# Optimization experiments

Measured on AMD Instinct MI355X. Metric: run time of the kernel, lower is better.

The kernel has to match this reference:

```python
import jax, jax.numpy as jnp
import numpy as np
import math

N, E, K_ORD = 30000, 60000, 6
D, H, DQK, PE_DIM, HYPER, MAX_K = 256, 8, 256, 128, 256, 10
DH = DQK // H    # per-head qk dim (dim_qk_head)
DVH = D // H     # per-head v dim  (dim_v_head)
M = E * K_ORD + N  # incidence messages + node self-loops


def _sin_pe(max_len, d):
    pos = np.arange(max_len)[:, None].astype(np.float32)
    div = np.exp(np.arange(0, d, 2).astype(np.float32) * (-math.log(10000.0) / d))
    pe = np.zeros((max_len, d), np.float32)
    pe[:, 0::2] = np.sin(pos * div)
    pe[:, 1::2] = np.cos(pos * div)
    return jnp.asarray(pe)


def _ln(x, g, b, eps=1e-5):
    mu = x.mean(-1, keepdims=True)
    var = ((x - mu) ** 2).mean(-1, keepdims=True)
    return (x - mu) * jax.lax.rsqrt(var + eps) * g + b


def _mlp(x, w1, b1, w2, b2):
    return jax.nn.relu(x @ w1 + b1) @ w2 + b2


def _forward(x_v, x_e, q_w1, q_b1, q_w2, q_b2, k_w, k_b, v_w, v_b,
             m1_w1, m1_b1, m1_w2, m1_b2, m2_w1, m2_b1, m2_w2, m2_b2,
             m3_w1, m3_b1, m3_w2, m3_b2, n1_g, n1_b, n2_g, n2_b, n3_g, n3_b,
             bias_v, edge_orders, edge_index):
    n = x_v.shape[0]
    # order-conditional positional MLP residual (pe1 at order 1 for nodes, edge_orders for edges)
    pe1 = _sin_pe(MAX_K + 1, D)
    x_v = x_v + _mlp(jnp.concatenate([_ln(x_v, n1_g, n1_b), jnp.broadcast_to(pe1[1], x_v.shape)], -1), m1_w1, m1_b1, m1_w2, m1_b2)
    x_e = x_e + _mlp(jnp.concatenate([_ln(x_e, n1_g, n1_b), pe1[edge_orders]], -1), m1_w1, m1_b1, m1_w2, m1_b2)

    # queries from PositionalMLP over positions {0, 1}
    q = _mlp(_sin_pe(2, PE_DIM), q_w1, q_b1, q_w2, q_b2)  # [2, DQK]
    q0 = q[0].reshape(H, DH)
    q1 = q[1].reshape(H, DH)

    tok = jnp.concatenate([x_e, x_v], 0)                    # [E+N, D], edges first
    k_all = tok @ k_w + k_b                                  # [E+N, 2*DQK]
    k0 = k_all[:, :DQK].reshape(-1, H, DH)
    k1 = k_all[:, DQK:].reshape(-1, H, DH)
    v = (tok @ v_w + v_b).reshape(-1, H, DVH)

    # global PMA: softmax over all edge+node tokens
    logit0 = jnp.einsum('hd,ehd->eh', q0, k0) / math.sqrt(DH)
    alpha0 = jax.nn.softmax(logit0, axis=0)
    att0 = jnp.einsum('eh,ehd->hd', alpha0, v).reshape(1, D)

    # segment PMA: leaky_relu -> scatter-softmax over messages per target node
    src, tgt = edge_index[0], edge_index[1]
    a = jnp.sum(k1 * q1[None], -1)                           # [E+N, H] (no sqrt scaling, per PMA)
    a = jax.nn.leaky_relu(a[src], 0.2)                       # [M, H]
    a_max = jax.ops.segment_max(a, tgt, num_segments=n)
    a = jnp.exp(a - a_max[tgt])
    a = a / jax.ops.segment_sum(a, tgt, num_segments=n)[tgt]
    att1 = jax.ops.segment_sum(v[src] * a[..., None], tgt, num_segments=n).reshape(n, D)

    pe2 = _sin_pe(2, D)
    att0 = att0 + _mlp(jnp.concatenate([_ln(att0, n2_g, n2_b), pe2[0:1]], -1), m2_w1, m2_b1, m2_w2, m2_b2)
    att1 = att1 + _mlp(jnp.concatenate([_ln(att1, n2_g, n2_b), jnp.broadcast_to(pe2[1], att1.shape)], -1), m2_w1, m2_b1, m2_w2, m2_b2)
    x = att0 + att1
    x = x + _mlp(_ln(x, n3_g, n3_b), m3_w1, m3_b1, m3_w2, m3_b2)
    return x + bias_v


def setup_inputs():
    key = jax.random.key(0)
    ks = jax.random.split(key, 64)
    idx = iter(range(64))
    def nrm(shape, fan_in=None):
        s = 1.0 if fan_in is None else 1.0 / math.sqrt(fan_in)
        return jax.random.normal(ks[next(idx)], shape, jnp.float32) * s
    inp = {}
    inp['x_v'] = nrm((N, D))
    inp['x_e'] = nrm((E, D))
    inp['edge_orders'] = jax.random.randint(ks[next(idx)], (E,), 2, MAX_K + 1)
    tgt_inc = jax.random.randint(ks[next(idx)], (E * K_ORD,), 0, N)
    src = jnp.concatenate([jnp.repeat(jnp.arange(E), K_ORD), E + jnp.arange(N)])
    tgt = jnp.concatenate([tgt_inc, jnp.arange(N)])
    inp['edge_index'] = jnp.stack([src, tgt]).astype(jnp.int32)
    inp['q_w1'] = nrm((PE_DIM, HYPER), PE_DIM); inp['q_b1'] = jnp.zeros((HYPER,), jnp.float32)
    inp['q_w2'] = nrm((HYPER, DQK), HYPER);     inp['q_b2'] = jnp.zeros((DQK,), jnp.float32)
    inp['k_w'] = nrm((D, 2 * DQK), D);          inp['k_b'] = jnp.zeros((2 * DQK,), jnp.float32)
    inp['v_w'] = nrm((D, D), D);                inp['v_b'] = jnp.zeros((D,), jnp.float32)
    inp['m1_w1'] = nrm((2 * D, HYPER), 2 * D);  inp['m1_b1'] = jnp.zeros((HYPER,), jnp.float32)
    inp['m1_w2'] = nrm((HYPER, D), HYPER);      inp['m1_b2'] = jnp.zeros((D,), jnp.float32)
    inp['m2_w1'] = nrm((2 * D, HYPER), 2 * D);  inp['m2_b1'] = jnp.zeros((HYPER,), jnp.float32)
    inp['m2_w2'] = nrm((HYPER, D), HYPER);      inp['m2_b2'] = jnp.zeros((D,), jnp.float32)
    inp['m3_w1'] = nrm((D, HYPER), D);          inp['m3_b1'] = jnp.zeros((HYPER,), jnp.float32)
    inp['m3_w2'] = nrm((HYPER, D), HYPER);      inp['m3_b2'] = jnp.zeros((D,), jnp.float32)
    for nm in ('n1', 'n2', 'n3'):
        inp[nm + '_g'] = jnp.ones((D,), jnp.float32)
        inp[nm + '_b'] = jnp.zeros((D,), jnp.float32)
    inp['bias_v'] = jnp.zeros((D,), jnp.float32)
    return inp


def reference(x_v, x_e, edge_orders, edge_index, q_w1, q_b1, q_w2, q_b2, k_w, k_b, v_w, v_b,
              m1_w1, m1_b1, m1_w2, m1_b2, m2_w1, m2_b1, m2_w2, m2_b2,
              m3_w1, m3_b1, m3_w2, m3_b2, n1_g, n1_b, n2_g, n2_b, n3_g, n3_b, bias_v):
    return _forward(x_v, x_e, q_w1, q_b1, q_w2, q_b2, k_w, k_b, v_w, v_b,
                    m1_w1, m1_b1, m1_w2, m1_b2, m2_w1, m2_b1, m2_w2, m2_b2,
                    m3_w1, m3_b1, m3_w2, m3_b2, n1_g, n1_b, n2_g, n2_b, n3_g, n3_b,
                    bias_v, edge_orders, edge_index)
```

## Files before the change

kernel.cpp:

```cpp
#include <hip/hip_runtime.h>
#include <hip/hip_bf16.h>

#define N_NODES 30000
#define N_EDGE  60000
#define T_TOK   90000
#define M_MSG   390000
#define DD      256
#define HH      8
#define AS      260
#define A0_BLOCKS 2048
#define A0_ROWS   44
#define FUSED_BLKS 1407
#define HIST_BLKS  762

typedef unsigned short u16;
typedef unsigned int   u32;
typedef short s16x8 __attribute__((ext_vector_type(8)));
typedef float f32x4 __attribute__((ext_vector_type(4)));

constexpr size_t WS_TOK   = 0;
constexpr size_t WS_V     = WS_TOK  + (size_t)T_TOK * DD * 2;
constexpr size_t WS_LOG0  = WS_V    + (size_t)T_TOK * DD * 2;
constexpr size_t WS_ALR   = WS_LOG0 + (size_t)T_TOK * HH * 4;
constexpr size_t WS_CNT   = WS_ALR  + (size_t)T_TOK * HH * 4;
constexpr size_t WS_OFF   = WS_CNT  + (size_t)N_NODES * 4;
constexpr size_t WS_CUR   = WS_OFF  + (size_t)(N_NODES + 1) * 4;
constexpr size_t WS_MSRC  = WS_CUR  + (size_t)N_NODES * 4;
constexpr size_t WS_SMALL = ((WS_MSRC + (size_t)M_MSG * 4) + 255) & ~(size_t)255;

struct Small {
  u16 wts[16][256];
  float b0[8], b1f[8];
  float q[2][256];
  float pe_c1[11][256];
  float pc2[2][256];
  int   gmaxi[8];
  float att0_vec[256];
  float att0_upd[256];
};
constexpr size_t WS_WTS  = (WS_SMALL + sizeof(Small) + 255) & ~(size_t)255;
constexpr size_t WS_PART = WS_WTS + 7 * 65536 * 2;
constexpr size_t WS_PDEN = WS_PART + (size_t)A0_BLOCKS * 256 * 4;

__device__ __forceinline__ float bf2f(u16 a){ return __uint_as_float(((u32)a) << 16); }
__device__ __forceinline__ u32 pkbf(float lo, float hi){
  u32 r;
  asm("v_cvt_pk_bf16_f32 %0, %1, %2" : "=v"(r) : "v"(lo), "v"(hi));
  return r;
}
__device__ __forceinline__ u16 f2bf(float f){ return (u16)pkbf(f, f); }
__device__ __forceinline__ float wredsum(float x){
  #pragma unroll
  for (int s = 32; s > 0; s >>= 1) x += __shfl_xor(x, s, 64);
  return x;
}
__device__ __forceinline__ u32 fenc(float f){
  u32 u = __float_as_uint(f);
  return (u & 0x80000000u) ? ~u : (u | 0x80000000u);
}
__device__ __forceinline__ float fdec(u32 k){
  return __uint_as_float((k & 0x80000000u) ? (k ^ 0x80000000u) : ~k);
}

union U8 { s16x8 v; uint2 u2[2]; uint4 u4; };

template<bool SC>
__device__ __forceinline__ void mfma_tile64(const u16* sa, const u16* __restrict__ WT,
                                            const u16* __restrict__ wts, int tid,
                                            f32x4 fr[4][2], f32x4* fs)
{
  const int lane = tid & 63, w = tid >> 6;
  const int l15 = lane & 15, g = lane >> 4;
  const int slab = w >> 1, nt0 = (w & 1) * 2;
  #pragma unroll
  for (int m = 0; m < 4; m++)
    #pragma unroll
    for (int n = 0; n < 2; n++) fr[m][n] = (f32x4){0.f, 0.f, 0.f, 0.f};
  const u16* ap = sa + l15 * AS + 4 * g;
  const u16* bp = WT + (size_t)slab * 16384 + lane * 8;
  const bool do_s = SC && (w == 0);
  #pragma unroll 4
  for (int c = 0; c < 8; c++){
    const int k0 = c * 32;
    U8 a[4];
    #pragma unroll
    for (int m = 0; m < 4; m++){
      a[m].u2[0] = *(const uint2*)(ap + m * 16 * AS + k0);
      a[m].u2[1] = *(const uint2*)(ap + m * 16 * AS + k0 + 16);
    }
    U8 b[2];
    #pragma unroll
    for (int n = 0; n < 2; n++)
      b[n].u4 = *(const uint4*)(bp + (c * 4 + nt0 + n) * 512);
    #pragma unroll
    for (int n = 0; n < 2; n++)
      #pragma unroll
      for (int m = 0; m < 4; m++)
        fr[m][n] = __builtin_amdgcn_mfma_f32_16x16x32_bf16(a[m].v, b[n].v, fr[m][n], 0, 0, 0);
    if (do_s){
      U8 bs;
      bs.u4 = *(const uint4*)(wts + c * 512 + lane * 8);
      #pragma unroll
      for (int m = 0; m < 4; m++)
        fs[m] = __builtin_amdgcn_mfma_f32_16x16x32_bf16(a[m].v, bs.v, fs[m], 0, 0, 0);
    }
  }
}

__global__ void k_preq(const float* __restrict__ qw1, const float* __restrict__ qb1,
                       const float* __restrict__ qw2, const float* __restrict__ qb2,
                       const float* __restrict__ kb, Small* sm, int* cnt)
{
  __shared__ float s_qin[2][128];
  __shared__ float s_h1[2][256];
  __shared__ float s_q[2][256];
  int tid = threadIdx.x;
  int p = tid >> 8, col = tid & 255;
  for (int i = tid; i < N_NODES; i += 512) cnt[i] = 0;
  if (tid < 8) ((u32*)sm->gmaxi)[tid] = 0u;
  if (tid < 128){
    int i = tid >> 1;
    float dv = expf((float)(2 * i) * (-9.210340371976184f / 128.f));
    if (tid & 1){ s_qin[0][tid] = 1.f; s_qin[1][tid] = cosf(dv); }
    else        { s_qin[0][tid] = 0.f; s_qin[1][tid] = sinf(dv); }
  }
  __syncthreads();
  {
    float acc = qb1[col];
    for (int d = 0; d < 128; d++) acc = fmaf(s_qin[p][d], qw1[d * 256 + col], acc);
    s_h1[p][col] = fmaxf(acc, 0.f);
  }
  __syncthreads();
  {
    float acc = qb2[col];
    for (int k = 0; k < 256; k++) acc = fmaf(s_h1[p][k], qw2[k * 256 + col], acc);
    s_q[p][col] = acc;
    sm->q[p][col] = acc;
  }
  __syncthreads();
  if (tid < 8){
    float b0 = 0.f, b1 = 0.f;
    for (int i = 0; i < 32; i++){
      b0 = fmaf(kb[tid * 32 + i],       s_q[0][tid * 32 + i], b0);
      b1 = fmaf(kb[256 + tid * 32 + i], s_q[1][tid * 32 + i], b1);
    }
    sm->b0[tid] = b0; sm->b1f[tid] = b1;
  }
}

__global__ void k_prew(const float* __restrict__ kw, const float* __restrict__ m1w1,
                       const float* __restrict__ m2w1, Small* sm)
{
  int role = blockIdx.x, tid = threadIdx.x;
  if (role < 8){
    int d = role * 32 + (tid >> 3), h = tid & 7;
    float a0 = 0.f, a1 = 0.f;
    #pragma unroll
    for (int i = 0; i < 32; i++){
      a0 = fmaf(kw[d * 512 + h * 32 + i],       sm->q[0][h * 32 + i], a0);
      a1 = fmaf(kw[d * 512 + 256 + h * 32 + i], sm->q[1][h * 32 + i], a1);
    }
    int c = d >> 5, kk = d & 31;
    int g = (kk & 15) >> 2;
    int j = (kk & 3) + ((kk & 16) ? 4 : 0);
    u16* wf = &sm->wts[0][0];
    wf[(c * 64 + g * 16 + h) * 8 + j]     = f2bf(a0);
    wf[(c * 64 + g * 16 + 8 + h) * 8 + j] = f2bf(a1);
  } else if (role < 19){
    __shared__ float s_pe[256];
    int o = role - 8;
    {
      int i = tid >> 1;
      float dv = expf((float)(2 * i) * (-9.210340371976184f / 256.f));
      float ph = (float)o * dv;
      s_pe[tid] = (tid & 1) ? cosf(ph) : sinf(ph);
    }
    __syncthreads();
    float acc = 0.f;
    for (int d = 0; d < 256; d++) acc = fmaf(s_pe[d], m1w1[(256 + d) * 256 + tid], acc);
    sm->pe_c1[o][tid] = acc;
  } else {
    __shared__ float p0[256], p1[256];
    {
      int i = tid >> 1;
      float dv = expf((float)(2 * i) * (-9.210340371976184f / 256.f));
      p0[tid] = (tid & 1) ? 1.f : 0.f;
      p1[tid] = (tid & 1) ? cosf(dv) : sinf(dv);
    }
    __syncthreads();
    float a0 = 0.f, a1 = 0.f;
    for (int d = 0; d < 256; d++){
      float w = m2w1[(256 + d) * 256 + tid];
      a0 = fmaf(p0[d], w, a0);
      a1 = fmaf(p1[d], w, a1);
    }
    sm->pc2[0][tid] = a0; sm->pc2[1][tid] = a1;
  }
}

__global__ void k_wconv(const float* __restrict__ s0, const float* __restrict__ s1,
                        const float* __restrict__ s2, const float* __restrict__ s3,
                        const float* __restrict__ s4, const float* __restrict__ s5,
                        const float* __restrict__ s6, u16* __restrict__ dst)
{
  int b = blockIdx.x;
  int mat = b >> 5, rem = b & 31;
  int slab = rem >> 3, c = rem & 7;
  const float* S;
  switch (mat){ case 0: S = s0; break; case 1: S = s1; break; case 2: S = s2; break;
                case 3: S = s3; break; case 4: S = s4; break; case 5: S = s5; break;
                default: S = s6; }
  int t = threadIdx.x;
  int nt = t >> 6, lane = t & 63;
  int l15 = lane & 15, g = lane >> 4;
  int n = slab * 64 + nt * 16 + l15;
  u16 tmp[8];
  #pragma unroll
  for (int j = 0; j < 8; j++){
    int k = c * 32 + g * 4 + (j & 3) + ((j >= 4) ? 16 : 0);
    tmp[j] = f2bf(S[(size_t)k * 256 + n]);
  }
  uint4 o;
  o.x = (u32)tmp[0] | ((u32)tmp[1] << 16);
  o.y = (u32)tmp[2] | ((u32)tmp[3] << 16);
  o.z = (u32)tmp[4] | ((u32)tmp[5] << 16);
  o.w = (u32)tmp[6] | ((u32)tmp[7] << 16);
  *(uint4*)(dst + (size_t)mat * 65536 + (size_t)((((slab * 8 + c) * 4 + nt) * 64 + lane) * 8)) = o;
}

__global__ __launch_bounds__(512, 4) void k_fused1(
    const float* __restrict__ x_v, const float* __restrict__ x_e,
    const int* __restrict__ edge_orders,
    const u16* __restrict__ WTa, const u16* __restrict__ WTb, const u16* __restrict__ WTv,
    const float* __restrict__ b1, const float* __restrict__ b2,
    const float* __restrict__ n1g, const float* __restrict__ n1b,
    const float* __restrict__ vb,
    Small* sm,
    u16* __restrict__ v, float* __restrict__ logit0, float* __restrict__ alr,
    const int* __restrict__ tgt, int* __restrict__ cnt)
{
  if (blockIdx.x >= FUSED_BLKS){
    int m = (blockIdx.x - FUSED_BLKS) * 512 + threadIdx.x;
    if (m < M_MSG) atomicAdd(&cnt[tgt[m]], 1);
    return;
  }
  __shared__ u16 s_a[64 * AS];
  __shared__ int s_ord[64];
  const int tid = threadIdx.x;
  const int t0  = blockIdx.x * 64;
  const int w = tid >> 6, lane = tid & 63;
  const int l15 = lane & 15, g = lane >> 4;
  const int cb = w * 32;

  uint2 xp[8];
  {
    float4 gg = *(const float4*)(n1g + lane * 4);
    float4 bb = *(const float4*)(n1b + lane * 4);
    #pragma unroll
    for (int i = 0; i < 8; i++){
      int r = w * 8 + i;
      int t = t0 + r;
      float4 xv = make_float4(0.f, 0.f, 0.f, 0.f);
      if (t < T_TOK){
        const float* p = (t < N_EDGE) ? (x_e + (size_t)t * DD) : (x_v + (size_t)(t - N_EDGE) * DD);
        xv = *(const float4*)(p + lane * 4);
      }
      xp[i].x = pkbf(xv.x, xv.y);
      xp[i].y = pkbf(xv.z, xv.w);
      float s  = xv.x + xv.y + xv.z + xv.w;
      float ss = fmaf(xv.x, xv.x, fmaf(xv.y, xv.y, fmaf(xv.z, xv.z, xv.w * xv.w)));
      s = wredsum(s); ss = wredsum(ss);
      float mu  = s * (1.f / 256.f);
      float var = fmaf(-mu, mu, ss * (1.f / 256.f));
      float rs  = rsqrtf(var + 1e-5f);
      uint2 p2;
      p2.x = pkbf(fmaf((xv.x - mu) * rs, gg.x, bb.x), fmaf((xv.y - mu) * rs, gg.y, bb.y));
      p2.y = pkbf(fmaf((xv.z - mu) * rs, gg.z, bb.z), fmaf((xv.w - mu) * rs, gg.w, bb.w));
      *(uint2*)(s_a + r * AS + lane * 4) = p2;
    }
  }
  if (tid < 64){
    int t = t0 + tid;
    s_ord[tid] = (t < N_EDGE) ? edge_orders[t] : 1;
  }
  __syncthreads();

  f32x4 fr[4][2];
  mfma_tile64<false>(s_a, WTa, nullptr, tid, fr, nullptr);
  __syncthreads();
  {
    float b1c[2];
    #pragma unroll
    for (int n = 0; n < 2; n++) b1c[n] = b1[cb + n * 16 + l15];
    #pragma unroll
    for (int m = 0; m < 4; m++){
      #pragma unroll
      for (int r = 0; r < 4; r++){
        int row = m * 16 + 4 * g + r;
        const float* per = &sm->pe_c1[s_ord[row]][0];
        #pragma unroll
        for (int n = 0; n < 2; n++){
          int col = cb + n * 16 + l15;
          s_a[row * AS + col] = f2bf(fmaxf(fr[m][n][r] + b1c[n] + per[col], 0.f));
        }
      }
    }
  }
  __syncthreads();
  mfma_tile64<false>(s_a, WTb, nullptr, tid, fr, nullptr);
  __syncthreads();
  {
    float b2c[2];
    #pragma unroll
    for (int n = 0; n < 2; n++) b2c[n] = b2[cb + n * 16 + l15];
    #pragma unroll
    for (int m = 0; m < 4; m++)
      #pragma unroll
      for (int n = 0; n < 2; n++){
        int col = cb + n * 16 + l15;
        #pragma unroll
        for (int r = 0; r < 4; r++){
          int row = m * 16 + 4 * g + r;
          s_a[row * AS + col] = f2bf(fr[m][n][r] + b2c[n]);
        }
      }
  }
  __syncthreads();
  #pragma unroll
  for (int i = 0; i < 8; i++){
    int r = w * 8 + i;
    uint2 q = *(const uint2*)(s_a + r * AS + lane * 4);
    uint2 xq = xp[i];
    uint2 o;
    o.x = pkbf(bf2f((u16)(q.x & 0xffff)) + bf2f((u16)(xq.x & 0xffff)),
               bf2f((u16)(q.x >> 16))    + bf2f((u16)(xq.x >> 16)));
    o.y = pkbf(bf2f((u16)(q.y & 0xffff)) + bf2f((u16)(xq.y & 0xffff)),
               bf2f((u16)(q.y >> 16))    + bf2f((u16)(xq.y >> 16)));
    *(uint2*)(s_a + r * AS + lane * 4) = o;
  }
  __syncthreads();
  f32x4 fs[4];
  #pragma unroll
  for (int m = 0; m < 4; m++) fs[m] = (f32x4){0.f, 0.f, 0.f, 0.f};
  mfma_tile64<true>(s_a, WTv, &sm->wts[0][0], tid, fr, fs);
  __syncthreads();
  {
    float vbc[2];
    #pragma unroll
    for (int n = 0; n < 2; n++) vbc[n] = vb[cb + n * 16 + l15];
    #pragma unroll
    for (int m = 0; m < 4; m++)
      #pragma unroll
      for (int n = 0; n < 2; n++){
        int col = cb + n * 16 + l15;
        #pragma unroll
        for (int r = 0; r < 4; r++){
          int row = m * 16 + 4 * g + r;
          s_a[row * AS + col] = f2bf(fr[m][n][r] + vbc[n]);
        }
      }
  }
  if (w == 0){
    float mx = -1e30f;
    #pragma unroll
    for (int m = 0; m < 4; m++)
      #pragma unroll
      for (int r = 0; r < 4; r++){
        int row = m * 16 + 4 * g + r;
        int t = t0 + row;
        int sc = l15;
        if (sc < 8){
          float lv = (fs[m][r] + sm->b0[sc]) * 0.17677669529663687f;
          mx = fmaxf(mx, lv);
          if (t < T_TOK) logit0[(size_t)t * 8 + sc] = lv;
        } else if (t < T_TOK){
          float a_ = fs[m][r] + sm->b1f[sc - 8];
          alr[(size_t)t * 8 + sc - 8] = (a_ > 0.f) ? a_ : 0.2f * a_;
        }
      }
    mx = fmaxf(mx, __shfl_xor(mx, 16, 64));
    mx = fmaxf(mx, __shfl_xor(mx, 32, 64));
    if (l15 < 8 && g == 0) atomicMax((u32*)&sm->gmaxi[l15], fenc(mx));
  }
  __syncthreads();
  #pragma unroll
  for (int i = 0; i < 4; i++){
    int ch = i * 512 + tid;
    int r = ch >> 5, c8 = (ch & 31) * 8;
    int t = t0 + r;
    if (t < T_TOK){
      uint2 q0 = *(const uint2*)(s_a + r * AS + c8);
      uint2 q1 = *(const uint2*)(s_a + r * AS + c8 + 4);
      *(uint4*)(v + (size_t)t * DD + c8) = make_uint4(q0.x, q0.y, q1.x, q1.y);
    }
  }
}

__global__ __launch_bounds__(256) void k_att0a(
    const float* __restrict__ logit0, const u16* __restrict__ v,
    const Small* __restrict__ sm, float* __restrict__ part, float* __restrict__ pden)
{
  __shared__ float s_part[8][256];
  __shared__ float s_den[8][8];
  int tid = threadIdx.x, b = blockIdx.x;
  int start = b * A0_ROWS;
  int end = min(start + A0_ROWS, T_TOK);
  int col8 = (tid & 31) * 8;
  int h = (tid & 31) >> 2;
  int rg = tid >> 5;
  float gm = fdec(((const u32*)sm->gmaxi)[h]);
  f32x4 a0 = {0.f, 0.f, 0.f, 0.f}, a1 = {0.f, 0.f, 0.f, 0.f};
  float aden = 0.f;
  for (int r = start + rg; r < end; r += 8){
    float al = __expf(logit0[(size_t)r * 8 + h] - gm);
    aden += al;
    uint4 raw = *(const uint4*)(v + (size_t)r * DD + col8);
    a0.x = fmaf(al, bf2f((u16)(raw.x & 0xffff)), a0.x);
    a0.y = fmaf(al, bf2f((u16)(raw.x >> 16)),    a0.y);
    a0.z = fmaf(al, bf2f((u16)(raw.y & 0xffff)), a0.z);
    a0.w = fmaf(al, bf2f((u16)(raw.y >> 16)),    a0.w);
    a1.x = fmaf(al, bf2f((u16)(raw.z & 0xffff)), a1.x);
    a1.y = fmaf(al, bf2f((u16)(raw.z >> 16)),    a1.y);
    a1.z = fmaf(al, bf2f((u16)(raw.w & 0xffff)), a1.z);
    a1.w = fmaf(al, bf2f((u16)(raw.w >> 16)),    a1.w);
  }
  *(f32x4*)&s_part[rg][col8]     = a0;
  *(f32x4*)&s_part[rg][col8 + 4] = a1;
  if ((tid & 3) == 0) s_den[rg][h] = aden;
  __syncthreads();
  float s = 0.f;
  #pragma unroll
  for (int g2 = 0; g2 < 8; g2++) s += s_part[g2][tid];
  part[(size_t)b * 256 + tid] = s;
  if (tid < 8){
    float d = 0.f;
    #pragma unroll
    for (int g2 = 0; g2 < 8; g2++) d += s_den[g2][tid];
    pden[(size_t)b * 8 + tid] = d;
  }
}

__global__ __launch_bounds__(1024) void k_att0bc(
    const float* __restrict__ part, const float* __restrict__ pden,
    const float* __restrict__ m2w1, const float* __restrict__ m2b1,
    const float* __restrict__ m2w2, const float* __restrict__ m2b2,
    const float* __restrict__ n2g, const float* __restrict__ n2b,
    Small* sm)
{
  __shared__ float s_acc[4][256];
  __shared__ float s_red[256];
  __shared__ float s_gi[8];
  __shared__ float s_ln[256], s_h[256], s_r2[8];
  int tid = threadIdx.x;
  if (tid < 256){
    int h = tid & 7, bi = tid >> 3;
    float s = 0.f;
    #pragma unroll 4
    for (int j = 0; j < 64; j++) s += pden[(size_t)(bi + 32 * j) * 8 + h];
    s_red[tid] = s;
  }
  __syncthreads();
  for (int s = 128; s >= 8; s >>= 1){ if (tid < s) s_red[tid] += s_red[tid + s]; __syncthreads(); }
  if (tid < 8) s_gi[tid] = 1.f / s_red[tid];
  {
    int col = tid & 255, bg = tid >> 8;
    float s = 0.f;
    #pragma unroll 4
    for (int b = bg * 512; b < (bg + 1) * 512; b++) s += part[(size_t)b * 256 + col];
    s_acc[bg][col] = s;
  }
  __syncthreads();
  float x = 0.f;
  if (tid < 256){
    x = (s_acc[0][tid] + s_acc[1][tid] + s_acc[2][tid] + s_acc[3][tid]) * s_gi[tid >> 5];
    sm->att0_vec[tid] = x;
  }
  float s1 = 0.f, s2 = 0.f;
  if (tid < 256){ s1 = wredsum(x); s2 = wredsum(x * x); }
  if (tid < 256 && (tid & 63) == 0){ s_r2[tid >> 6] = s1; s_r2[4 + (tid >> 6)] = s2; }
  __syncthreads();
  if (tid < 256){
    float tot  = s_r2[0] + s_r2[1] + s_r2[2] + s_r2[3];
    float tot2 = s_r2[4] + s_r2[5] + s_r2[6] + s_r2[7];
    float mu  = tot * (1.f / 256.f);
    float var = tot2 * (1.f / 256.f) - mu * mu;
    float rs  = rsqrtf(var + 1e-5f);
    s_ln[tid] = (x - mu) * rs * n2g[tid] + n2b[tid];
  }
  __syncthreads();
  {
    int col = tid & 255, kg = tid >> 8;
    float acc = 0.f;
    for (int k = kg * 64; k < (kg + 1) * 64; k++) acc = fmaf(s_ln[k], m2w1[k * 256 + col], acc);
    s_acc[kg][col] = acc;
  }
  __syncthreads();
  if (tid < 256){
    float acc = s_acc[0][tid] + s_acc[1][tid] + s_acc[2][tid] + s_acc[3][tid]
              + m2b1[tid] + sm->pc2[0][tid];
    s_h[tid] = fmaxf(acc, 0.f);
  }
  __syncthreads();
  {
    int col = tid & 255, kg = tid >> 8;
    float acc = 0.f;
    for (int k = kg * 64; k < (kg + 1) * 64; k++) acc = fmaf(s_h[k], m2w2[k * 256 + col], acc);
    s_acc[kg][col] = acc;
  }
  __syncthreads();
  if (tid < 256){
    sm->att0_upd[tid] = x + s_acc[0][tid] + s_acc[1][tid] + s_acc[2][tid] + s_acc[3][tid] + m2b2[tid];
  }
}

__global__ void k_scan(const int* __restrict__ cnt, int* __restrict__ off, int* __restrict__ cur){
  __shared__ int s_s[1024];
  int tid = threadIdx.x;
  int base = tid * 30;
  int s = 0;
  if (tid < 1000){
    for (int i = 0; i < 30; i++) s += cnt[base + i];
  }
  s_s[tid] = s;
  __syncthreads();
  for (int ofs = 1; ofs < 1024; ofs <<= 1){
    int v_ = (tid >= ofs) ? s_s[tid - ofs] : 0;
    __syncthreads();
    s_s[tid] += v_;
    __syncthreads();
  }
  if (tid < 1000){
    int run = (tid == 0) ? 0 : s_s[tid - 1];
    for (int i = 0; i < 30; i++){
      int c = cnt[base + i];
      off[base + i] = run; cur[base + i] = run;
      run += c;
    }
  }
  if (tid == 0) off[N_NODES] = M_MSG;
}

__global__ void k_scatter(const int* __restrict__ src, const int* __restrict__ tgt,
                          int* __restrict__ cur, int* __restrict__ msrc){
  int m = blockIdx.x * 256 + threadIdx.x;
  if (m < M_MSG){
    int slot = atomicAdd(&cur[tgt[m]], 1);
    msrc[slot] = src[m];
  }
}

__global__ __launch_bounds__(256) void k_att1(
    const int* __restrict__ off, const int* __restrict__ msrc,
    const float* __restrict__ alr, const u16* __restrict__ v,
    float* att1)
{
  int tid = threadIdx.x;
  int n = blockIdx.x * 4 + (tid >> 6);
  if (n >= N_NODES) return;
  int l = tid & 63;
  int h = l >> 3;
  int beg = off[n], end = off[n + 1];
  float mxa = -1e30f, mxb = -1e30f;
  int i = beg;
  for (; i + 1 < end; i += 2){
    mxa = fmaxf(mxa, alr[(size_t)msrc[i] * 8 + h]);
    mxb = fmaxf(mxb, alr[(size_t)msrc[i + 1] * 8 + h]);
  }
  if (i < end) mxa = fmaxf(mxa, alr[(size_t)msrc[i] * 8 + h]);
  float mx = fmaxf(mxa, mxb);
  float den0 = 0.f, den1 = 0.f;
  float a0 = 0.f, a1 = 0.f, a2 = 0.f, a3 = 0.f;
  float c0 = 0.f, c1 = 0.f, c2 = 0.f, c3 = 0.f;
  i = beg;
  for (; i + 1 < end; i += 2){
    int s0 = msrc[i], s1 = msrc[i + 1];
    float w0 = __expf(alr[(size_t)s0 * 8 + h] - mx);
    float w1 = __expf(alr[(size_t)s1 * 8 + h] - mx);
    ushort4 r0 = *(const ushort4*)(v + (size_t)s0 * DD + l * 4);
    ushort4 r1 = *(const ushort4*)(v + (size_t)s1 * DD + l * 4);
    den0 += w0; den1 += w1;
    a0 = fmaf(w0, bf2f(r0.x), a0); c0 = fmaf(w1, bf2f(r1.x), c0);
    a1 = fmaf(w0, bf2f(r0.y), a1); c1 = fmaf(w1, bf2f(r1.y), c1);
    a2 = fmaf(w0, bf2f(r0.z), a2); c2 = fmaf(w1, bf2f(r1.z), c2);
    a3 = fmaf(w0, bf2f(r0.w), a3); c3 = fmaf(w1, bf2f(r1.w), c3);
  }
  if (i < end){
    int s0 = msrc[i];
    float w0 = __expf(alr[(size_t)s0 * 8 + h] - mx);
    ushort4 r0 = *(const ushort4*)(v + (size_t)s0 * DD + l * 4);
    den0 += w0;
    a0 = fmaf(w0, bf2f(r0.x), a0);
    a1 = fmaf(w0, bf2f(r0.y), a1);
    a2 = fmaf(w0, bf2f(r0.z), a2);
    a3 = fmaf(w0, bf2f(r0.w), a3);
  }
  float id_ = 1.f / (den0 + den1);
  *(float4*)(att1 + (size_t)n * DD + l * 4) =
      make_float4((a0 + c0) * id_, (a1 + c1) * id_, (a2 + c2) * id_, (a3 + c3) * id_);
}

__global__ __launch_bounds__(512, 4) void k_final(
    const float* att1,
    const u16* __restrict__ WT2a, const u16* __restrict__ WT2b,
    const u16* __restrict__ WT3a, const u16* __restrict__ WT3b,
    const float* __restrict__ m2b1, const float* __restrict__ m2b2,
    const float* __restrict__ m3b1, const float* __restrict__ m3b2,
    const float* __restrict__ n2g, const float* __restrict__ n2b,
    const float* __restrict__ n3g, const float* __restrict__ n3b,
    const float* __restrict__ bias_v, const Small* __restrict__ sm,
    float* out)
{
  __shared__ u16 s_a[64 * AS];
  const int tid = threadIdx.x;
  const int t0  = blockIdx.x * 64;
  const int w = tid >> 6, lane = tid & 63;
  const int l15 = lane & 15, g = lane >> 4;
  const int cb = w * 32;

  f32x4 xr[8];
  {
    float4 gg = *(const float4*)(n2g + lane * 4);
    float4 bb = *(const float4*)(n2b + lane * 4);
    #pragma unroll
    for (int i = 0; i < 8; i++){
      int r = w * 8 + i;
      int t = t0 + r;
      float4 xv = make_float4(0.f, 0.f, 0.f, 0.f);
      if (t < N_NODES) xv = *(const float4*)(att1 + (size_t)t * DD + lane * 4);
      xr[i][0] = xv.x; xr[i][1] = xv.y; xr[i][2] = xv.z; xr[i][3] = xv.w;
      float s  = xv.x + xv.y + xv.z + xv.w;
      float ss = fmaf(xv.x, xv.x, fmaf(xv.y, xv.y, fmaf(xv.z, xv.z, xv.w * xv.w)));
      s = wredsum(s); ss = wredsum(ss);
      float mu  = s * (1.f / 256.f);
      float var = fmaf(-mu, mu, ss * (1.f / 256.f));
      float rs  = rsqrtf(var + 1e-5f);
      uint2 p2;
      p2.x = pkbf(fmaf((xv.x - mu) * rs, gg.x, bb.x), fmaf((xv.y - mu) * rs, gg.y, bb.y));
      p2.y = pkbf(fmaf((xv.z - mu) * rs, gg.z, bb.z), fmaf((xv.w - mu) * rs, gg.w, bb.w));
      *(uint2*)(s_a + r * AS + lane * 4) = p2;
    }
  }
  __syncthreads();

  f32x4 fr[4][2];
  mfma_tile64<false>(s_a, WT2a, nullptr, tid, fr, nullptr);
  __syncthreads();
  {
    float bc[2], pc[2];
    #pragma unroll
    for (int n = 0; n < 2; n++){
      int col = cb + n * 16 + l15;
      bc[n] = m2b1[col]; pc[n] = sm->pc2[1][col];
    }
    #pragma unroll
    for (int m = 0; m < 4; m++)
      #pragma unroll
      for (int n = 0; n < 2; n++){
        int col = cb + n * 16 + l15;
        #pragma unroll
        for (int r = 0; r < 4; r++){
          int row = m * 16 + 4 * g + r;
          s_a[row * AS + col] = f2bf(fmaxf(fr[m][n][r] + bc[n] + pc[n], 0.f));
        }
      }
  }
  __syncthreads();
  mfma_tile64<false>(s_a, WT2b, nullptr, tid, fr, nullptr);
  __syncthreads();
  {
    float bc[2], ac[2];
    #pragma unroll
    for (int n = 0; n < 2; n++){
      int col = cb + n * 16 + l15;
      bc[n] = m2b2[col]; ac[n] = sm->att0_upd[col];
    }
    #pragma unroll
    for (int m = 0; m < 4; m++)
      #pragma unroll
      for (int n = 0; n < 2; n++){
        int col = cb + n * 16 + l15;
        #pragma unroll
        for (int r = 0; r < 4; r++){
          int row = m * 16 + 4 * g + r;
          s_a[row * AS + col] = f2bf(fr[m][n][r] + bc[n] + ac[n]);
        }
      }
  }
  __syncthreads();
  {
    float4 gg = *(const float4*)(n3g + lane * 4);
    float4 bb = *(const float4*)(n3b + lane * 4);
    #pragma unroll
    for (int i = 0; i < 8; i++){
      int r = w * 8 + i;
      uint2 q = *(const uint2*)(s_a + r * AS + lane * 4);
      float x0 = xr[i][0] + bf2f((u16)(q.x & 0xffff));
      float x1 = xr[i][1] + bf2f((u16)(q.x >> 16));
      float x2 = xr[i][2] + bf2f((u16)(q.y & 0xffff));
      float x3 = xr[i][3] + bf2f((u16)(q.y >> 16));
      xr[i][0] = x0; xr[i][1] = x1; xr[i][2] = x2; xr[i][3] = x3;
      float s  = x0 + x1 + x2 + x3;
      float ss = fmaf(x0, x0, fmaf(x1, x1, fmaf(x2, x2, x3 * x3)));
      s = wredsum(s); ss = wredsum(ss);
      float mu  = s * (1.f / 256.f);
      float var = fmaf(-mu, mu, ss * (1.f / 256.f));
      float rs  = rsqrtf(var + 1e-5f);
      uint2 p2;
      p2.x = pkbf(fmaf((x0 - mu) * rs, gg.x, bb.x), fmaf((x1 - mu) * rs, gg.y, bb.y));
      p2.y = pkbf(fmaf((x2 - mu) * rs, gg.z, bb.z), fmaf((x3 - mu) * rs, gg.w, bb.w));
      *(uint2*)(s_a + r * AS + lane * 4) = p2;
    }
  }
  __syncthreads();
  mfma_tile64<false>(s_a, WT3a, nullptr, tid, fr, nullptr);
  __syncthreads();
  {
    float bc[2];
    #pragma unroll
    for (int n = 0; n < 2; n++) bc[n] = m3b1[cb + n * 16 + l15];
    #pragma unroll
    for (int m = 0; m < 4; m++)
      #pragma unroll
      for (int n = 0; n < 2; n++){
        int col = cb + n * 16 + l15;
        #pragma unroll
        for (int r = 0; r < 4; r++){
          int row = m * 16 + 4 * g + r;
          s_a[row * AS + col] = f2bf(fmaxf(fr[m][n][r] + bc[n], 0.f));
        }
      }
  }
  __syncthreads();
  mfma_tile64<false>(s_a, WT3b, nullptr, tid, fr, nullptr);
  __syncthreads();
  {
    float bc[2];
    #pragma unroll
    for (int n = 0; n < 2; n++){
      int col = cb + n * 16 + l15;
      bc[n] = m3b2[col] + bias_v[col];
    }
    #pragma unroll
    for (int m = 0; m < 4; m++)
      #pragma unroll
      for (int n = 0; n < 2; n++){
        int col = cb + n * 16 + l15;
        #pragma unroll
        for (int r = 0; r < 4; r++){
          int row = m * 16 + 4 * g + r;
          s_a[row * AS + col] = f2bf(fr[m][n][r] + bc[n]);
        }
      }
  }
  __syncthreads();
  #pragma unroll
  for (int i = 0; i < 8; i++){
    int r = w * 8 + i;
    int t = t0 + r;
    if (t < N_NODES){
      uint2 q = *(const uint2*)(s_a + r * AS + lane * 4);
      float4 o;
      o.x = xr[i][0] + bf2f((u16)(q.x & 0xffff));
      o.y = xr[i][1] + bf2f((u16)(q.x >> 16));
      o.z = xr[i][2] + bf2f((u16)(q.y & 0xffff));
      o.w = xr[i][3] + bf2f((u16)(q.y >> 16));
      *(float4*)(out + (size_t)t * DD + lane * 4) = o;
    }
  }
}

extern "C" void kernel_launch(void* const* d_in, const int* in_sizes, int n_in,
                              void* d_out, int out_size, void* d_ws, size_t ws_size,
                              hipStream_t stream)
{
  const float* x_v = (const float*)d_in[0];
  const float* x_e = (const float*)d_in[1];
  const int* edge_orders = (const int*)d_in[2];
  const int* edge_index  = (const int*)d_in[3];
  const float* q_w1 = (const float*)d_in[4],  *q_b1 = (const float*)d_in[5];
  const float* q_w2 = (const float*)d_in[6],  *q_b2 = (const float*)d_in[7];
  const float* k_w  = (const float*)d_in[8],  *k_b  = (const float*)d_in[9];
  const float* v_w  = (const float*)d_in[10], *v_b  = (const float*)d_in[11];
  const float* m1w1 = (const float*)d_in[12], *m1b1 = (const float*)d_in[13];
  const float* m1w2 = (const float*)d_in[14], *m1b2 = (const float*)d_in[15];
  const float* m2w1 = (const float*)d_in[16], *m2b1 = (const float*)d_in[17];
  const float* m2w2 = (const float*)d_in[18], *m2b2 = (const float*)d_in[19];
  const float* m3w1 = (const float*)d_in[20], *m3b1 = (const float*)d_in[21];
  const float* m3w2 = (const float*)d_in[22], *m3b2 = (const float*)d_in[23];
  const float* n1g = (const float*)d_in[24], *n1b = (const float*)d_in[25];
  const float* n2g = (const float*)d_in[26], *n2b = (const float*)d_in[27];
  const float* n3g = (const float*)d_in[28], *n3b = (const float*)d_in[29];
  const float* bias_v = (const float*)d_in[30];

  char* ws = (char*)d_ws;
  u16*   v      = (u16*)  (ws + WS_V);
  float* logit0 = (float*)(ws + WS_LOG0);
  float* alr    = (float*)(ws + WS_ALR);
  int*   cnt    = (int*)  (ws + WS_CNT);
  int*   off    = (int*)  (ws + WS_OFF);
  int*   cur    = (int*)  (ws + WS_CUR);
  int*   msrc   = (int*)  (ws + WS_MSRC);
  Small* sm     = (Small*)(ws + WS_SMALL);
  u16*   wtb    = (u16*)  (ws + WS_WTS);
  float* part   = (float*)(ws + WS_PART);
  float* pden   = (float*)(ws + WS_PDEN);
  const int* src = edge_index;
  const int* tgt = edge_index + M_MSG;
  float* att1 = (float*)d_out;
  float* out  = (float*)d_out;

  k_preq<<<1, 512, 0, stream>>>(q_w1, q_b1, q_w2, q_b2, k_b, sm, cnt);
  k_prew<<<20, 256, 0, stream>>>(k_w, m1w1, m2w1, sm);
  k_wconv<<<224, 256, 0, stream>>>(m1w1, m1w2, v_w, m2w1, m2w2, m3w1, m3w2, wtb);
  k_fused1<<<FUSED_BLKS + HIST_BLKS, 512, 0, stream>>>(x_v, x_e, edge_orders,
                                                  wtb + 0 * 65536, wtb + 1 * 65536, wtb + 2 * 65536,
                                                  m1b1, m1b2, n1g, n1b, v_b, sm, v, logit0, alr,
                                                  tgt, cnt);
  k_scan<<<1, 1024, 0, stream>>>(cnt, off, cur);
  k_scatter<<<(M_MSG + 255) / 256, 256, 0, stream>>>(src, tgt, cur, msrc);
  k_att0a<<<A0_BLOCKS, 256, 0, stream>>>(logit0, v, sm, part, pden);
  k_att0bc<<<1, 1024, 0, stream>>>(part, pden, m2w1, m2b1, m2w2, m2b2, n2g, n2b, sm);
  k_att1<<<(N_NODES + 3) / 4, 256, 0, stream>>>(off, msrc, alr, v, att1);
  k_final<<<(N_NODES + 63) / 64, 512, 0, stream>>>(att1,
                                                   wtb + 3 * 65536, wtb + 4 * 65536,
                                                   wtb + 5 * 65536, wtb + 6 * 65536,
                                                   m2b1, m2b2, m3b1, m3b2,
                                                   n2g, n2b, n3g, n3b, bias_v, sm, out);
}
```

Measured before the change: 301.2 us.

## Fuse global softmax-attention partials into projection kernel with per-block max rescaling

The global PMA attention is now computed inside the fused projection kernel. Each block finds its own per-head max, sums the exponentials, and forms a weighted V partial from the shared-memory tile. This removes the global atomicMax, the logit0 buffer, and the separate k_att0a pass that re-read all of V. The reduction kernel rescales the partials by exp(block max − global max) and is merged with the scan into a two-block launch, and the weight-conversion kernel is merged into the prep kernel. Together this cuts the launch count and the V reread, at the cost of more shared memory and extra work in the already heavy fused kernel.

```diff
diff --git a/kernel.cpp b/kernel.cpp
--- a/kernel.cpp
+++ b/kernel.cpp
@@ -8,8 +8,6 @@
 #define DD      256
 #define HH      8
 #define AS      260
-#define A0_BLOCKS 2048
-#define A0_ROWS   44
 #define FUSED_BLKS 1407
 #define HIST_BLKS  762
 
@@ -18,10 +16,8 @@
 typedef short s16x8 __attribute__((ext_vector_type(8)));
 typedef float f32x4 __attribute__((ext_vector_type(4)));
 
-constexpr size_t WS_TOK   = 0;
-constexpr size_t WS_V     = WS_TOK  + (size_t)T_TOK * DD * 2;
-constexpr size_t WS_LOG0  = WS_V    + (size_t)T_TOK * DD * 2;
-constexpr size_t WS_ALR   = WS_LOG0 + (size_t)T_TOK * HH * 4;
+constexpr size_t WS_V     = 0;
+constexpr size_t WS_ALR   = WS_V    + (size_t)T_TOK * DD * 2;
 constexpr size_t WS_CNT   = WS_ALR  + (size_t)T_TOK * HH * 4;
 constexpr size_t WS_OFF   = WS_CNT  + (size_t)N_NODES * 4;
 constexpr size_t WS_CUR   = WS_OFF  + (size_t)(N_NODES + 1) * 4;
@@ -34,13 +30,13 @@
   float q[2][256];
   float pe_c1[11][256];
   float pc2[2][256];
-  int   gmaxi[8];
   float att0_vec[256];
   float att0_upd[256];
 };
 constexpr size_t WS_WTS  = (WS_SMALL + sizeof(Small) + 255) & ~(size_t)255;
-constexpr size_t WS_PART = WS_WTS + 7 * 65536 * 2;
-constexpr size_t WS_PDEN = WS_PART + (size_t)A0_BLOCKS * 256 * 4;
+constexpr size_t WS_PART = WS_WTS  + 7 * 65536 * 2;
+constexpr size_t WS_PDEN = WS_PART + (size_t)FUSED_BLKS * 256 * 4;
+constexpr size_t WS_PMAX = WS_PDEN + (size_t)FUSED_BLKS * 8 * 4;
 
 __device__ __forceinline__ float bf2f(u16 a){ return __uint_as_float(((u32)a) << 16); }
 __device__ __forceinline__ u32 pkbf(float lo, float hi){
@@ -54,12 +50,10 @@
   for (int s = 32; s > 0; s >>= 1) x += __shfl_xor(x, s, 64);
   return x;
 }
-__device__ __forceinline__ u32 fenc(float f){
-  u32 u = __float_as_uint(f);
-  return (u & 0x80000000u) ? ~u : (u | 0x80000000u);
-}
-__device__ __forceinline__ float fdec(u32 k){
-  return __uint_as_float((k & 0x80000000u) ? (k ^ 0x80000000u) : ~k);
+__device__ __forceinline__ float wredmax(float x){
+  #pragma unroll
+  for (int s = 32; s > 0; s >>= 1) x = fmaxf(x, __shfl_xor(x, s, 64));
+  return x;
 }
 
 union U8 { s16x8 v; uint2 u2[2]; uint4 u4; };
@@ -117,7 +111,6 @@
   int tid = threadIdx.x;
   int p = tid >> 8, col = tid & 255;
   for (int i = tid; i < N_NODES; i += 512) cnt[i] = 0;
-  if (tid < 8) ((u32*)sm->gmaxi)[tid] = 0u;
   if (tid < 128){
     int i = tid >> 1;
     float dv = expf((float)(2 * i) * (-9.210340371976184f / 128.f));
@@ -148,8 +141,12 @@
   }
 }
 
-__global__ void k_prew(const float* __restrict__ kw, const float* __restrict__ m1w1,
-                       const float* __restrict__ m2w1, Small* sm)
+__global__ void k_prep(const float* __restrict__ kw, const float* __restrict__ m1w1,
+                       const float* __restrict__ m2w1, Small* sm,
+                       const float* __restrict__ s0, const float* __restrict__ s1,
+                       const float* __restrict__ s2, const float* __restrict__ s3,
+                       const float* __restrict__ s4, const float* __restrict__ s5,
+                       const float* __restrict__ s6, u16* __restrict__ dst)
 {
   int role = blockIdx.x, tid = threadIdx.x;
   if (role < 8){
@@ -179,7 +176,7 @@
     float acc = 0.f;
     for (int d = 0; d < 256; d++) acc = fmaf(s_pe[d], m1w1[(256 + d) * 256 + tid], acc);
     sm->pe_c1[o][tid] = acc;
-  } else {
+  } else if (role == 19){
     __shared__ float p0[256], p1[256];
     {
       int i = tid >> 1;
@@ -195,37 +192,30 @@
       a1 = fmaf(p1[d], w, a1);
     }
     sm->pc2[0][tid] = a0; sm->pc2[1][tid] = a1;
-  }
-}
-
-__global__ void k_wconv(const float* __restrict__ s0, const float* __restrict__ s1,
-                        const float* __restrict__ s2, const float* __restrict__ s3,
-                        const float* __restrict__ s4, const float* __restrict__ s5,
-                        const float* __restrict__ s6, u16* __restrict__ dst)
-{
-  int b = blockIdx.x;
-  int mat = b >> 5, rem = b & 31;
-  int slab = rem >> 3, c = rem & 7;
-  const float* S;
-  switch (mat){ case 0: S = s0; break; case 1: S = s1; break; case 2: S = s2; break;
-                case 3: S = s3; break; case 4: S = s4; break; case 5: S = s5; break;
-                default: S = s6; }
-  int t = threadIdx.x;
-  int nt = t >> 6, lane = t & 63;
-  int l15 = lane & 15, g = lane >> 4;
-  int n = slab * 64 + nt * 16 + l15;
-  u16 tmp[8];
-  #pragma unroll
-  for (int j = 0; j < 8; j++){
-    int k = c * 32 + g * 4 + (j & 3) + ((j >= 4) ? 16 : 0);
-    tmp[j] = f2bf(S[(size_t)k * 256 + n]);
-  }
-  uint4 o;
-  o.x = (u32)tmp[0] | ((u32)tmp[1] << 16);
-  o.y = (u32)tmp[2] | ((u32)tmp[3] << 16);
-  o.z = (u32)tmp[4] | ((u32)tmp[5] << 16);
-  o.w = (u32)tmp[6] | ((u32)tmp[7] << 16);
-  *(uint4*)(dst + (size_t)mat * 65536 + (size_t)((((slab * 8 + c) * 4 + nt) * 64 + lane) * 8)) = o;
+  } else {
+    int b = role - 20;
+    int mat = b >> 5, rem = b & 31;
+    int slab = rem >> 3, c = rem & 7;
+    const float* S;
+    switch (mat){ case 0: S = s0; break; case 1: S = s1; break; case 2: S = s2; break;
+                  case 3: S = s3; break; case 4: S = s4; break; case 5: S = s5; break;
+                  default: S = s6; }
+    int nt = tid >> 6, lane = tid & 63;
+    int l15 = lane & 15, g = lane >> 4;
+    int n = slab * 64 + nt * 16 + l15;
+    u16 tmp[8];
+    #pragma unroll
+    for (int j = 0; j < 8; j++){
+      int k = c * 32 + g * 4 + (j & 3) + ((j >= 4) ? 16 : 0);
+      tmp[j] = f2bf(S[(size_t)k * 256 + n]);
+    }
+    uint4 o;
+    o.x = (u32)tmp[0] | ((u32)tmp[1] << 16);
+    o.y = (u32)tmp[2] | ((u32)tmp[3] << 16);
+    o.z = (u32)tmp[4] | ((u32)tmp[5] << 16);
+    o.w = (u32)tmp[6] | ((u32)tmp[7] << 16);
+    *(uint4*)(dst + (size_t)mat * 65536 + (size_t)((((slab * 8 + c) * 4 + nt) * 64 + lane) * 8)) = o;
+  }
 }
 
 __global__ __launch_bounds__(512, 4) void k_fused1(
@@ -235,8 +225,9 @@
     const float* __restrict__ b1, const float* __restrict__ b2,
     const float* __restrict__ n1g, const float* __restrict__ n1b,
     const float* __restrict__ vb,
-    Small* sm,
-    u16* __restrict__ v, float* __restrict__ logit0, float* __restrict__ alr,
+    const Small* __restrict__ sm,
+    u16* __restrict__ v, float* __restrict__ alr,
+    float* __restrict__ part, float* __restrict__ pden, float* __restrict__ pmax,
     const int* __restrict__ tgt, int* __restrict__ cnt)
 {
   if (blockIdx.x >= FUSED_BLKS){
@@ -246,6 +237,9 @@
   }
   __shared__ u16 s_a[64 * AS];
   __shared__ int s_ord[64];
+  __shared__ float s_l[64][8];
+  __shared__ float s_e[8][64];
+  __shared__ float s_p2[512];
   const int tid = threadIdx.x;
   const int t0  = blockIdx.x * 64;
   const int w = tid >> 6, lane = tid & 63;
@@ -361,7 +355,6 @@
       }
   }
   if (w == 0){
-    float mx = -1e30f;
     #pragma unroll
     for (int m = 0; m < 4; m++)
       #pragma unroll
@@ -370,19 +363,38 @@
         int t = t0 + row;
         int sc = l15;
         if (sc < 8){
-          float lv = (fs[m][r] + sm->b0[sc]) * 0.17677669529663687f;
-          mx = fmaxf(mx, lv);
-          if (t < T_TOK) logit0[(size_t)t * 8 + sc] = lv;
+          float lv = (t < T_TOK) ? (fs[m][r] + sm->b0[sc]) * 0.17677669529663687f : -1e30f;
+          s_l[row][sc] = lv;
         } else if (t < T_TOK){
           float a_ = fs[m][r] + sm->b1f[sc - 8];
           alr[(size_t)t * 8 + sc - 8] = (a_ > 0.f) ? a_ : 0.2f * a_;
         }
       }
-    mx = fmaxf(mx, __shfl_xor(mx, 16, 64));
-    mx = fmaxf(mx, __shfl_xor(mx, 32, 64));
-    if (l15 < 8 && g == 0) atomicMax((u32*)&sm->gmaxi[l15], fenc(mx));
-  }
-  __syncthreads();
+  }
+  __syncthreads();
+  {
+    float lv = s_l[lane][w];
+    float mxb = wredmax(lv);
+    float e = __expf(lv - mxb);
+    float den = wredsum(e);
+    s_e[w][lane] = e;
+    if (lane == 0){
+      pden[(size_t)blockIdx.x * 8 + w] = den;
+      pmax[(size_t)blockIdx.x * 8 + w] = mxb;
+    }
+  }
+  __syncthreads();
+  {
+    int col = tid & 255, half = tid >> 8;
+    int h = col >> 5;
+    float acc = 0.f;
+    #pragma unroll 8
+    for (int r2 = half * 32; r2 < half * 32 + 32; r2++)
+      acc = fmaf(s_e[h][r2], bf2f(s_a[r2 * AS + col]), acc);
+    s_p2[tid] = acc;
+  }
+  __syncthreads();
+  if (tid < 256) part[(size_t)blockIdx.x * 256 + tid] = s_p2[tid] + s_p2[tid + 256];
   #pragma unroll
   for (int i = 0; i < 4; i++){
     int ch = i * 512 + tid;
@@ -396,77 +408,74 @@
   }
 }
 
-__global__ __launch_bounds__(256) void k_att0a(
-    const float* __restrict__ logit0, const u16* __restrict__ v,
-    const Small* __restrict__ sm, float* __restrict__ part, float* __restrict__ pden)
-{
-  __shared__ float s_part[8][256];
-  __shared__ float s_den[8][8];
-  int tid = threadIdx.x, b = blockIdx.x;
-  int start = b * A0_ROWS;
-  int end = min(start + A0_ROWS, T_TOK);
-  int col8 = (tid & 31) * 8;
-  int h = (tid & 31) >> 2;
-  int rg = tid >> 5;
-  float gm = fdec(((const u32*)sm->gmaxi)[h]);
-  f32x4 a0 = {0.f, 0.f, 0.f, 0.f}, a1 = {0.f, 0.f, 0.f, 0.f};
-  float aden = 0.f;
-  for (int r = start + rg; r < end; r += 8){
-    float al = __expf(logit0[(size_t)r * 8 + h] - gm);
-    aden += al;
-    uint4 raw = *(const uint4*)(v + (size_t)r * DD + col8);
-    a0.x = fmaf(al, bf2f((u16)(raw.x & 0xffff)), a0.x);
-    a0.y = fmaf(al, bf2f((u16)(raw.x >> 16)),    a0.y);
-    a0.z = fmaf(al, bf2f((u16)(raw.y & 0xffff)), a0.z);
-    a0.w = fmaf(al, bf2f((u16)(raw.y >> 16)),    a0.w);
-    a1.x = fmaf(al, bf2f((u16)(raw.z & 0xffff)), a1.x);
-    a1.y = fmaf(al, bf2f((u16)(raw.z >> 16)),    a1.y);
-    a1.z = fmaf(al, bf2f((u16)(raw.w & 0xffff)), a1.z);
-    a1.w = fmaf(al, bf2f((u16)(raw.w >> 16)),    a1.w);
-  }
-  *(f32x4*)&s_part[rg][col8]     = a0;
-  *(f32x4*)&s_part[rg][col8 + 4] = a1;
-  if ((tid & 3) == 0) s_den[rg][h] = aden;
-  __syncthreads();
-  float s = 0.f;
-  #pragma unroll
-  for (int g2 = 0; g2 < 8; g2++) s += s_part[g2][tid];
-  part[(size_t)b * 256 + tid] = s;
-  if (tid < 8){
-    float d = 0.f;
-    #pragma unroll
-    for (int g2 = 0; g2 < 8; g2++) d += s_den[g2][tid];
-    pden[(size_t)b * 8 + tid] = d;
-  }
-}
-
-__global__ __launch_bounds__(1024) void k_att0bc(
-    const float* __restrict__ part, const float* __restrict__ pden,
+__global__ __launch_bounds__(1024) void k_scanbc(
+    const int* __restrict__ cnt, int* __restrict__ off, int* __restrict__ cur,
+    const float* __restrict__ part, const float* __restrict__ pden, const float* __restrict__ pmax,
     const float* __restrict__ m2w1, const float* __restrict__ m2b1,
     const float* __restrict__ m2w2, const float* __restrict__ m2b2,
     const float* __restrict__ n2g, const float* __restrict__ n2b,
     Small* sm)
 {
+  int tid = threadIdx.x;
+  if (blockIdx.x == 0){
+    __shared__ int s_s[1024];
+    int base = tid * 30;
+    int s = 0;
+    if (tid < 1000){
+      for (int i = 0; i < 30; i++) s += cnt[base + i];
+    }
+    s_s[tid] = s;
+    __syncthreads();
+    for (int ofs = 1; ofs < 1024; ofs <<= 1){
+      int v_ = (tid >= ofs) ? s_s[tid - ofs] : 0;
+      __syncthreads();
+      s_s[tid] += v_;
+      __syncthreads();
+    }
+    if (tid < 1000){
+      int run = (tid == 0) ? 0 : s_s[tid - 1];
+      for (int i = 0; i < 30; i++){
+        int c = cnt[base + i];
+        off[base + i] = run; cur[base + i] = run;
+        run += c;
+      }
+    }
+    if (tid == 0) off[N_NODES] = M_MSG;
+    return;
+  }
   __shared__ float s_acc[4][256];
   __shared__ float s_red[256];
-  __shared__ float s_gi[8];
+  __shared__ float s_g[8], s_gi[8];
   __shared__ float s_ln[256], s_h[256], s_r2[8];
-  int tid = threadIdx.x;
   if (tid < 256){
     int h = tid & 7, bi = tid >> 3;
+    float m = -1e30f;
+    for (int b = bi; b < FUSED_BLKS; b += 32) m = fmaxf(m, pmax[(size_t)b * 8 + h]);
+    s_red[tid] = m;
+  }
+  __syncthreads();
+  for (int s = 128; s >= 8; s >>= 1){ if (tid < s) s_red[tid] = fmaxf(s_red[tid], s_red[tid + s]); __syncthreads(); }
+  if (tid < 8) s_g[tid] = s_red[tid];
+  __syncthreads();
+  if (tid < 256){
+    int h = tid & 7, bi = tid >> 3;
+    float gm = s_g[h];
     float s = 0.f;
-    #pragma unroll 4
-    for (int j = 0; j < 64; j++) s += pden[(size_t)(bi + 32 * j) * 8 + h];
+    for (int b = bi; b < FUSED_BLKS; b += 32)
+      s += pden[(size_t)b * 8 + h] * __expf(pmax[(size_t)b * 8 + h] - gm);
     s_red[tid] = s;
   }
   __syncthreads();
   for (int s = 128; s >= 8; s >>= 1){ if (tid < s) s_red[tid] += s_red[tid + s]; __syncthreads(); }
   if (tid < 8) s_gi[tid] = 1.f / s_red[tid];
+  __syncthreads();
   {
     int col = tid & 255, bg = tid >> 8;
+    int h = col >> 5;
+    float gm = s_g[h];
     float s = 0.f;
-    #pragma unroll 4
-    for (int b = bg * 512; b < (bg + 1) * 512; b++) s += part[(size_t)b * 256 + col];
+    for (int b = bg; b < FUSED_BLKS; b += 4)
+      s += part[(size_t)b * 256 + col] * __expf(pmax[(size_t)b * 8 + h] - gm);
     s_acc[bg][col] = s;
   }
   __syncthreads();
@@ -511,33 +520,6 @@
   if (tid < 256){
     sm->att0_upd[tid] = x + s_acc[0][tid] + s_acc[1][tid] + s_acc[2][tid] + s_acc[3][tid] + m2b2[tid];
   }
-}
-
-__global__ void k_scan(const int* __restrict__ cnt, int* __restrict__ off, int* __restrict__ cur){
-  __shared__ int s_s[1024];
-  int tid = threadIdx.x;
-  int base = tid * 30;
-  int s = 0;
-  if (tid < 1000){
-    for (int i = 0; i < 30; i++) s += cnt[base + i];
-  }
-  s_s[tid] = s;
-  __syncthreads();
-  for (int ofs = 1; ofs < 1024; ofs <<= 1){
-    int v_ = (tid >= ofs) ? s_s[tid - ofs] : 0;
-    __syncthreads();
-    s_s[tid] += v_;
-    __syncthreads();
-  }
-  if (tid < 1000){
-    int run = (tid == 0) ? 0 : s_s[tid - 1];
-    for (int i = 0; i < 30; i++){
-      int c = cnt[base + i];
-      off[base + i] = run; cur[base + i] = run;
-      run += c;
-    }
-  }
-  if (tid == 0) off[N_NODES] = M_MSG;
 }
 
 __global__ void k_scatter(const int* __restrict__ src, const int* __restrict__ tgt,
@@ -794,7 +776,6 @@
 
   char* ws = (char*)d_ws;
   u16*   v      = (u16*)  (ws + WS_V);
-  float* logit0 = (float*)(ws + WS_LOG0);
   float* alr    = (float*)(ws + WS_ALR);
   int*   cnt    = (int*)  (ws + WS_CNT);
   int*   off    = (int*)  (ws + WS_OFF);
@@ -804,22 +785,22 @@
   u16*   wtb    = (u16*)  (ws + WS_WTS);
   float* part   = (float*)(ws + WS_PART);
   float* pden   = (float*)(ws + WS_PDEN);
+  float* pmax   = (float*)(ws + WS_PMAX);
   const int* src = edge_index;
   const int* tgt = edge_index + M_MSG;
   float* att1 = (float*)d_out;
   float* out  = (float*)d_out;
 
   k_preq<<<1, 512, 0, stream>>>(q_w1, q_b1, q_w2, q_b2, k_b, sm, cnt);
-  k_prew<<<20, 256, 0, stream>>>(k_w, m1w1, m2w1, sm);
-  k_wconv<<<224, 256, 0, stream>>>(m1w1, m1w2, v_w, m2w1, m2w2, m3w1, m3w2, wtb);
+  k_prep<<<244, 256, 0, stream>>>(k_w, m1w1, m2w1, sm,
+                                  m1w1, m1w2, v_w, m2w1, m2w2, m3w1, m3w2, wtb);
   k_fused1<<<FUSED_BLKS + HIST_BLKS, 512, 0, stream>>>(x_v, x_e, edge_orders,
                                                   wtb + 0 * 65536, wtb + 1 * 65536, wtb + 2 * 65536,
-                                                  m1b1, m1b2, n1g, n1b, v_b, sm, v, logit0, alr,
-                                                  tgt, cnt);
-  k_scan<<<1, 1024, 0, stream>>>(cnt, off, cur);
+                                                  m1b1, m1b2, n1g, n1b, v_b, sm, v, alr,
+                                                  part, pden, pmax, tgt, cnt);
+  k_scanbc<<<2, 1024, 0, stream>>>(cnt, off, cur, part, pden, pmax,
+                                   m2w1, m2b1, m2w2, m2b2, n2g, n2b, sm);
   k_scatter<<<(M_MSG + 255) / 256, 256, 0, stream>>>(src, tgt, cur, msrc);
-  k_att0a<<<A0_BLOCKS, 256, 0, stream>>>(logit0, v, sm, part, pden);
-  k_att0bc<<<1, 1024, 0, stream>>>(part, pden, m2w1, m2b1, m2w2, m2b2, n2g, n2b, sm);
   k_att1<<<(N_NODES + 3) / 4, 256, 0, stream>>>(off, msrc, alr, v, att1);
   k_final<<<(N_NODES + 63) / 64, 512, 0, stream>>>(att1,
                                                    wtb + 3 * 65536, wtb + 4 * 65536,
```

Result: slower. 347.1 us (+15.2%).
